# Performance work log

Measured on AMD Instinct MI355X. Metric: run time of the kernel, lower is better.

The kernel has to match this reference:

```python
import jax, jax.numpy as jnp
import numpy as np
import math

D_MODEL = 1024
NUM_HEADS = 16
D_K = D_MODEL // NUM_HEADS  # 64
THETA = 10000.0
B, S = 2, 2048


def setup_inputs() -> dict:
    key = jax.random.key(0)
    kx, kq, kk, kv, ko = jax.random.split(key, 5)
    sigma = (2.0 / (D_MODEL + D_MODEL)) ** 0.5
    return {
        "x": jax.random.normal(kx, (B, S, D_MODEL), dtype=jnp.float32),
        "Wq": jax.random.normal(kq, (D_MODEL, D_MODEL), dtype=jnp.float32) * sigma,
        "Wk": jax.random.normal(kk, (D_MODEL, D_MODEL), dtype=jnp.float32) * sigma,
        "Wv": jax.random.normal(kv, (D_MODEL, D_MODEL), dtype=jnp.float32) * sigma,
        "Wo": jax.random.normal(ko, (D_MODEL, D_MODEL), dtype=jnp.float32) * sigma,
        "token_positions": jnp.arange(S, dtype=jnp.int32),
    }


def _rope(x, token_positions):
    # x: [..., seq, d_k]; rotate interleaved even/odd pairs.
    half = x.shape[-1] // 2
    freq = jnp.power(THETA, -jnp.arange(0, x.shape[-1], 2, dtype=jnp.float32) / x.shape[-1])  # [half]
    angles = token_positions[:, None].astype(jnp.float32) * freq[None, :]  # [seq, half]
    cos, sin = jnp.cos(angles), jnp.sin(angles)
    x1 = x[..., 0::2]
    x2 = x[..., 1::2]
    out = jnp.stack([x1 * cos - x2 * sin, x1 * sin + x2 * cos], axis=-1)  # [..., seq, half, 2]
    return out.reshape(x.shape)


def reference(x, Wq, Wk, Wv, Wo, token_positions):
    Bb, Ss, Dm = x.shape
    H, Dk = NUM_HEADS, D_K
    # Linear: y = x @ W.T ; split as (n head) -> heads first
    def heads(y):
        return y.reshape(Bb, Ss, H, Dk).transpose(0, 2, 1, 3)  # [B,H,S,Dk]
    Q = heads(x @ Wq.T)
    K = heads(x @ Wk.T)
    V = heads(x @ Wv.T)
    Q = _rope(Q, token_positions)
    K = _rope(K, token_positions)
    scores = jnp.einsum("bhqd,bhkd->bhqk", Q, K) / math.sqrt(Dk)  # [B,H,S,S]
    causal = jnp.tril(jnp.ones((Ss, Ss), dtype=bool))
    scores = jnp.where(causal, scores, -jnp.inf)
    # original casts to fp64 for softmax; numerically-stable fp32 softmax here
    probs = jax.nn.softmax(scores, axis=-1)
    attn = jnp.einsum("bhqk,bhkd->bhqd", probs, V)  # [B,H,S,Dk]
    attn = attn.transpose(0, 2, 1, 3).reshape(Bb, Ss, Dm)
    return attn @ Wo.T
```

## Files before the change

kernel.cpp:

```cpp
#include <hip/hip_runtime.h>
#include <hip/hip_bf16.h>
#include <math.h>

typedef __bf16 bf16_t;
typedef __attribute__((ext_vector_type(8))) __bf16 bf16x8;
typedef __attribute__((ext_vector_type(4))) __bf16 bf16x4;
typedef __attribute__((ext_vector_type(4))) float f32x4;

#define B_DIM 2
#define S_DIM 2048
#define H_DIM 16
#define DK 64
#define DM 1024
#define KDIM 1024

#define MFMA(a, b, c) __builtin_amdgcn_mfma_f32_16x16x32_bf16((a), (b), (c), 0, 0, 0)

__device__ __forceinline__ void gload_lds16(const bf16_t* g, bf16_t* l) {
    __builtin_amdgcn_global_load_lds(
        (const __attribute__((address_space(1))) void*)g,
        (__attribute__((address_space(3))) void*)l, 16, 0, 0);
}

__global__ void cvt_all(const float* __restrict__ x,
                        const float* __restrict__ wq, const float* __restrict__ wk,
                        const float* __restrict__ wv, const float* __restrict__ wo,
                        bf16_t* __restrict__ xb,
                        bf16_t* __restrict__ wqb, bf16_t* __restrict__ wkb,
                        bf16_t* __restrict__ wvb, bf16_t* __restrict__ wob) {
    const long NX = (long)B_DIM * S_DIM * DM;
    const long i = ((long)blockIdx.x * 256 + threadIdx.x) * 4;
    const float* s; bf16_t* d; long off;
    if (i < NX) { s = x; d = xb; off = i; }
    else {
        const long j = i - NX;
        const int wsel = (int)(j >> 20);
        off = j & ((1L << 20) - 1);
        switch (wsel) {
            case 0: s = wq; d = wqb; break;
            case 1: s = wk; d = wkb; break;
            case 2: s = wv; d = wvb; break;
            default: s = wo; d = wob; break;
        }
    }
    float4 v = *reinterpret_cast<const float4*>(s + off);
    bf16x4 o;
    o[0] = (__bf16)v.x; o[1] = (__bf16)v.y; o[2] = (__bf16)v.z; o[3] = (__bf16)v.w;
    *reinterpret_cast<bf16x4*>(d + off) = o;
}

template <int MODE>
__global__ __launch_bounds__(256)
void gemm_bt(const bf16_t* __restrict__ A,
             const bf16_t* __restrict__ B0,
             const bf16_t* __restrict__ B1,
             const bf16_t* __restrict__ B2,
             bf16_t* __restrict__ outQ,
             bf16_t* __restrict__ outK,
             bf16_t* __restrict__ outVt,
             float* __restrict__ outF,
             const int* __restrict__ pos) {
    constexpr int CP = 136;
    constexpr int SELEMS = (MODE == 0) ? (128 * CP) : 16384;
    __shared__ bf16_t smem[SELEMS];
    bf16_t* As = smem;
    bf16_t* Bs = smem + 8192;
    bf16_t* Cs = smem;

    const int t = threadIdx.x;
    const int z = blockIdx.z;
    const bf16_t* Bm = (MODE == 0) ? (z == 0 ? B0 : (z == 1 ? B1 : B2)) : B0;

    const int m0 = blockIdx.x * 128;
    const int n0 = blockIdx.y * 128;
    const int lane = t & 63;
    const int w = t >> 6;
    const int wr = w >> 1;
    const int wc = w & 1;

    f32x4 acc[4][4] = {};

    const bf16_t* Ag = A + (size_t)m0 * KDIM;
    const bf16_t* Bg = Bm + (size_t)n0 * KDIM;

    const int rr = lane & 15;
    const int ko = (lane >> 4) * 8;

    int rI[4], cI[4];
#pragma unroll
    for (int c = 0; c < 4; ++c) {
        const int i = t + c * 256;
        rI[c] = i >> 3;
        cI[c] = ((i & 7) ^ (rI[c] & 7)) * 8;
    }

    for (int k0 = 0; k0 < KDIM; k0 += 64) {
#pragma unroll
        for (int c = 0; c < 4; ++c) {
            const int i = t + c * 256;
            gload_lds16(Ag + (size_t)rI[c] * KDIM + k0 + cI[c], &As[i * 8]);
        }
#pragma unroll
        for (int c = 0; c < 4; ++c) {
            const int i = t + c * 256;
            gload_lds16(Bg + (size_t)rI[c] * KDIM + k0 + cI[c], &Bs[i * 8]);
        }
        __syncthreads();

        bf16x8 af[2][4], bfr[2][4];
#pragma unroll
        for (int kk = 0; kk < 2; ++kk) {
#pragma unroll
            for (int m = 0; m < 4; ++m) {
                const int r = wr * 64 + m * 16 + rr;
                af[kk][m] = *reinterpret_cast<const bf16x8*>(
                    &As[r * 64 + ((kk * 32 + ko) ^ ((r & 7) * 8))]);
            }
#pragma unroll
            for (int n = 0; n < 4; ++n) {
                const int r = wc * 64 + n * 16 + rr;
                bfr[kk][n] = *reinterpret_cast<const bf16x8*>(
                    &Bs[r * 64 + ((kk * 32 + ko) ^ ((r & 7) * 8))]);
            }
        }
        __builtin_amdgcn_s_setprio(1);
#pragma unroll
        for (int kk = 0; kk < 2; ++kk)
#pragma unroll
            for (int m = 0; m < 4; ++m)
#pragma unroll
                for (int n = 0; n < 4; ++n)
                    acc[m][n] = MFMA(af[kk][m], bfr[kk][n], acc[m][n]);
        __builtin_amdgcn_s_setprio(0);
        __syncthreads();
    }

    const int rlb = wr * 64 + (lane >> 4) * 4;
    const int clb = wc * 64 + (lane & 15);

    if (MODE == 0) {
        if (z < 2) {
#pragma unroll
            for (int m = 0; m < 4; ++m)
#pragma unroll
                for (int n = 0; n < 4; ++n)
#pragma unroll
                    for (int j = 0; j < 4; ++j)
                        Cs[(rlb + m * 16 + j) * CP + clb + n * 16] = (__bf16)acc[m][n][j];
            __syncthreads();

            bf16_t* dst = (z == 0) ? outQ : outK;
            const int dch = t & 7;
            const int srow = t >> 3;
            float fr[4];
#pragma unroll
            for (int i = 0; i < 4; ++i)
                fr[i] = exp2f((float)(dch * 4 + i) * -0.4152410118609203f);
#pragma unroll
            for (int p = 0; p < 4; ++p) {
                const int s_loc = p * 32 + srow;
                const int gm = m0 + s_loc;
                const int bb = gm >> 11, sg = gm & (S_DIM - 1);
                const float pv = (float)pos[sg];
                float csv[4], snv[4];
#pragma unroll
                for (int i = 0; i < 4; ++i) {
                    const float a = pv * fr[i];
                    csv[i] = cosf(a); snv[i] = sinf(a);
                }
#pragma unroll
                for (int hc = 0; hc < 2; ++hc) {
                    const bf16x8 vv = *reinterpret_cast<const bf16x8*>(
                        &Cs[s_loc * CP + hc * 64 + dch * 8]);
                    bf16x8 ov;
#pragma unroll
                    for (int i = 0; i < 4; ++i) {
                        const float v0 = (float)vv[2 * i], v1 = (float)vv[2 * i + 1];
                        ov[2 * i]     = (__bf16)(v0 * csv[i] - v1 * snv[i]);
                        ov[2 * i + 1] = (__bf16)(v0 * snv[i] + v1 * csv[i]);
                    }
                    const int h = (n0 >> 6) + hc;
                    *reinterpret_cast<bf16x8*>(
                        &dst[((size_t)(bb * H_DIM + h) * S_DIM + sg) * 64 + dch * 8]) = ov;
                }
            }
        } else {
#pragma unroll
            for (int m = 0; m < 4; ++m)
#pragma unroll
                for (int n = 0; n < 4; ++n) {
                    const int cl = clb + n * 16;
                    bf16x4 v4;
#pragma unroll
                    for (int j = 0; j < 4; ++j) v4[j] = (__bf16)acc[m][n][j];
                    *reinterpret_cast<bf16x4*>(&Cs[cl * CP + rlb + m * 16]) = v4;
                }
            __syncthreads();

            const int cl = t >> 1, sh = t & 1;
            const int cg = n0 + cl, h = cg >> 6, d = cg & 63;
            const int bb = m0 >> 11, s0g = m0 & (S_DIM - 1);
            bf16_t* vdst = &outVt[((size_t)(bb * H_DIM + h) * DK + d) * S_DIM + s0g + sh * 64];
#pragma unroll
            for (int i = 0; i < 8; ++i)
                *reinterpret_cast<bf16x8*>(&vdst[i * 8]) =
                    *reinterpret_cast<const bf16x8*>(&Cs[cl * CP + sh * 64 + i * 8]);
        }
    } else {
        const int rbase = m0 + rlb;
        const int cbase = n0 + clb;
#pragma unroll
        for (int m = 0; m < 4; ++m)
#pragma unroll
            for (int n = 0; n < 4; ++n)
#pragma unroll
                for (int j = 0; j < 4; ++j)
                    outF[(size_t)(rbase + m * 16 + j) * DM + cbase + n * 16] = acc[m][n][j];
    }
}

__global__ __launch_bounds__(512, 4)
void attn_kernel(const bf16_t* __restrict__ Q, const bf16_t* __restrict__ Kg,
                 const bf16_t* __restrict__ Vt, bf16_t* __restrict__ O) {
    constexpr int PSTR = 72;
    __shared__ bf16_t Ks[2][64 * 64];
    __shared__ bf16_t Vs[2][64 * 64];
    __shared__ bf16_t P_lds[8][16 * PSTR];

    const int t = threadIdx.x;
    const int lane = t & 63;
    const int w = t >> 6;
    const int bh = blockIdx.x >> 4;
    const int qi = blockIdx.x & 15;
    const int qbH = 31 - qi, qbL = qi;
    const int qbC = (w < 4) ? qbH : qbL;
    const int q0 = qbC * 64 + (w & 3) * 16;
    const int b = bh >> 4, h = bh & 15;
    const int rr = lane & 15;
    const int hi = lane >> 4;

    const bf16_t* Kbh = Kg + (size_t)bh * S_DIM * DK;
    const bf16_t* Vbh = Vt + (size_t)bh * DK * S_DIM;
    bf16_t* Pw = P_lds[w];

    const int r0 = t >> 3, c0 = ((t & 7) ^ (r0 & 7)) * 8;

    const float QSCALE = 0.18033688011112042f;
    const bf16_t* Qp = Q + ((size_t)bh * S_DIM + q0) * DK;
    bf16x8 qf[2];
    qf[0] = *reinterpret_cast<const bf16x8*>(&Qp[rr * DK + hi * 8]);
    qf[1] = *reinterpret_cast<const bf16x8*>(&Qp[rr * DK + 32 + hi * 8]);
#pragma unroll
    for (int i = 0; i < 8; ++i) {
        qf[0][i] = (__bf16)((float)qf[0][i] * QSCALE);
        qf[1][i] = (__bf16)((float)qf[1][i] * QSCALE);
    }

    bf16x8 ones;
#pragma unroll
    for (int i = 0; i < 8; ++i) ones[i] = (__bf16)1.0f;

    f32x4 o[4] = {};
    f32x4 la = {};
    float m = -INFINITY;

    const int ntH = qbH + 1;

    gload_lds16(Kbh + (size_t)r0 * DK + c0, &Ks[0][t * 8]);
    gload_lds16(Vbh + (size_t)r0 * S_DIM + c0, &Vs[0][t * 8]);
    __syncthreads();

    for (int tt = 0; tt < ntH; ++tt) {
        const int cur = tt & 1;
        const int kv0 = tt * 64;

        if (tt + 1 < ntH) {
            const int kv1 = kv0 + 64;
            gload_lds16(Kbh + (size_t)(kv1 + r0) * DK + c0, &Ks[cur ^ 1][t * 8]);
            gload_lds16(Vbh + (size_t)r0 * S_DIM + kv1 + c0, &Vs[cur ^ 1][t * 8]);
        }
        const bf16_t* Kc = Ks[cur];
        const bf16_t* Vc = Vs[cur];

        if (tt <= qbC) {
            f32x4 s[4] = {};
            __builtin_amdgcn_s_setprio(1);
#pragma unroll
            for (int t16 = 0; t16 < 4; ++t16) {
                const int r = t16 * 16 + rr;
                const int sw = (r & 7) * 8;
                bf16x8 kf0 = *reinterpret_cast<const bf16x8*>(&Kc[r * 64 + ((hi * 8) ^ sw)]);
                bf16x8 kf1 = *reinterpret_cast<const bf16x8*>(&Kc[r * 64 + ((32 + hi * 8) ^ sw)]);
                s[t16] = MFMA(kf0, qf[0], s[t16]);
                s[t16] = MFMA(kf1, qf[1], s[t16]);
            }
            __builtin_amdgcn_s_setprio(0);

            if (tt == qbC) {
                const int qg = q0 + rr;
#pragma unroll
                for (int t16 = 0; t16 < 4; ++t16)
#pragma unroll
                    for (int j = 0; j < 4; ++j)
                        if (kv0 + t16 * 16 + hi * 4 + j > qg) s[t16][j] = -INFINITY;
            }

            f32x4 mv = s[0];
#pragma unroll
            for (int t16 = 1; t16 < 4; ++t16) {
                mv[0] = fmaxf(mv[0], s[t16][0]); mv[1] = fmaxf(mv[1], s[t16][1]);
                mv[2] = fmaxf(mv[2], s[t16][2]); mv[3] = fmaxf(mv[3], s[t16][3]);
            }
            const float mloc = fmaxf(fmaxf(mv[0], mv[1]), fmaxf(mv[2], mv[3]));
            if (__any(mloc - m > 8.0f)) {
                float mf = fmaxf(mloc, __shfl_xor(mloc, 16));
                mf = fmaxf(mf, __shfl_xor(mf, 32));
                const float mnew = fmaxf(m, mf);
                const float scale = exp2f(m - mnew);
#pragma unroll
                for (int i = 0; i < 4; ++i) la[i] *= scale;
#pragma unroll
                for (int db = 0; db < 4; ++db)
#pragma unroll
                    for (int j = 0; j < 4; ++j) o[db][j] *= scale;
                m = mnew;
            }
#pragma unroll
            for (int t16 = 0; t16 < 4; ++t16) {
                bf16x4 pb;
#pragma unroll
                for (int j = 0; j < 4; ++j) pb[j] = (__bf16)exp2f(s[t16][j] - m);
                *reinterpret_cast<bf16x4*>(&Pw[rr * PSTR + t16 * 16 + hi * 4]) = pb;
            }

            bf16x8 pf0 = *reinterpret_cast<const bf16x8*>(&Pw[rr * PSTR + hi * 8]);
            bf16x8 pf1 = *reinterpret_cast<const bf16x8*>(&Pw[rr * PSTR + 32 + hi * 8]);
            __builtin_amdgcn_s_setprio(1);
            la = MFMA(ones, pf0, la);
            la = MFMA(ones, pf1, la);
#pragma unroll
            for (int db = 0; db < 4; ++db) {
                const int vr = db * 16 + rr;
                const int sw = (vr & 7) * 8;
                bf16x8 vf0 = *reinterpret_cast<const bf16x8*>(&Vc[vr * 64 + ((hi * 8) ^ sw)]);
                bf16x8 vf1 = *reinterpret_cast<const bf16x8*>(&Vc[vr * 64 + ((32 + hi * 8) ^ sw)]);
                o[db] = MFMA(vf0, pf0, o[db]);
                o[db] = MFMA(vf1, pf1, o[db]);
            }
            __builtin_amdgcn_s_setprio(0);
        }

        __syncthreads();
    }

    const float linv = 1.0f / la[0];
#pragma unroll
    for (int db = 0; db < 4; ++db) {
        bf16x4 ov;
#pragma unroll
        for (int j = 0; j < 4; ++j) ov[j] = (__bf16)(o[db][j] * linv);
        *reinterpret_cast<bf16x4*>(
            &O[((size_t)(b * S_DIM + q0 + rr)) * DM + h * DK + db * 16 + hi * 4]) = ov;
    }
}

extern "C" void kernel_launch(void* const* d_in, const int* in_sizes, int n_in,
                              void* d_out, int out_size, void* d_ws, size_t ws_size,
                              hipStream_t stream) {
    const float* x  = (const float*)d_in[0];
    const float* Wq = (const float*)d_in[1];
    const float* Wk = (const float*)d_in[2];
    const float* Wv = (const float*)d_in[3];
    const float* Wo = (const float*)d_in[4];
    const int* pos  = (const int*)d_in[5];
    float* out = (float*)d_out;

    char* ws = (char*)d_ws;
    bf16_t* xb  = (bf16_t*)(ws);
    bf16_t* Wqb = (bf16_t*)(ws + (8u << 20));
    bf16_t* Wkb = (bf16_t*)(ws + (10u << 20));
    bf16_t* Wvb = (bf16_t*)(ws + (12u << 20));
    bf16_t* Wob = (bf16_t*)(ws + (14u << 20));
    bf16_t* Qb  = (bf16_t*)(ws + (16u << 20));
    bf16_t* Kb  = (bf16_t*)(ws + (24u << 20));
    bf16_t* Vtb = (bf16_t*)(ws + (32u << 20));
    bf16_t* Ab  = (bf16_t*)(ws);

    const int NX = B_DIM * S_DIM * DM;
    const int NW = DM * DM;
    const int NTOT = NX + 4 * NW;

    cvt_all<<<NTOT / 1024, 256, 0, stream>>>(x, Wq, Wk, Wv, Wo,
                                             xb, Wqb, Wkb, Wvb, Wob);

    gemm_bt<0><<<dim3(32, 8, 3), 256, 0, stream>>>(xb, Wqb, Wkb, Wvb,
                                                   Qb, Kb, Vtb, nullptr, pos);

    attn_kernel<<<B_DIM * H_DIM * 16, 512, 0, stream>>>(Qb, Kb, Vtb, Ab);

    gemm_bt<1><<<dim3(32, 8, 1), 256, 0, stream>>>(Ab, Wob, nullptr, nullptr,
                                                   nullptr, nullptr, nullptr, out, pos);
}
```

Baseline: 113.9 us.

## Replace paired causal q-blocks with one q-block per 256-thread workgroup, heavy-first order

```diff
diff --git a/kernel.cpp b/kernel.cpp
--- a/kernel.cpp
+++ b/kernel.cpp
@@ -219,31 +219,32 @@
     }
 }
 
-__global__ __launch_bounds__(512, 4)
+__global__ __launch_bounds__(256, 4)
 void attn_kernel(const bf16_t* __restrict__ Q, const bf16_t* __restrict__ Kg,
                  const bf16_t* __restrict__ Vt, bf16_t* __restrict__ O) {
-    constexpr int PSTR = 72;
     __shared__ bf16_t Ks[2][64 * 64];
     __shared__ bf16_t Vs[2][64 * 64];
-    __shared__ bf16_t P_lds[8][16 * PSTR];
+    __shared__ bf16_t P_lds[4][16 * 64];
 
     const int t = threadIdx.x;
     const int lane = t & 63;
     const int w = t >> 6;
-    const int bh = blockIdx.x >> 4;
-    const int qi = blockIdx.x & 15;
-    const int qbH = 31 - qi, qbL = qi;
-    const int qbC = (w < 4) ? qbH : qbL;
-    const int q0 = qbC * 64 + (w & 3) * 16;
+    const int qbo = blockIdx.x >> 5;
+    const int qb = 31 - qbo;
+    const int bh = blockIdx.x & 31;
+    const int q0 = qb * 64 + w * 16;
     const int b = bh >> 4, h = bh & 15;
     const int rr = lane & 15;
     const int hi = lane >> 4;
+    const int psw = (rr & 7) * 8;
 
     const bf16_t* Kbh = Kg + (size_t)bh * S_DIM * DK;
     const bf16_t* Vbh = Vt + (size_t)bh * DK * S_DIM;
     bf16_t* Pw = P_lds[w];
 
-    const int r0 = t >> 3, c0 = ((t & 7) ^ (r0 & 7)) * 8;
+    const int i0 = t, i1 = t + 256;
+    const int r0 = i0 >> 3, c0 = ((i0 & 7) ^ (r0 & 7)) * 8;
+    const int r1 = i1 >> 3, c1 = ((i1 & 7) ^ (r1 & 7)) * 8;
 
     const float QSCALE = 0.18033688011112042f;
     const bf16_t* Qp = Q + ((size_t)bh * S_DIM + q0) * DK;
@@ -264,91 +265,95 @@
     f32x4 la = {};
     float m = -INFINITY;
 
-    const int ntH = qbH + 1;
-
-    gload_lds16(Kbh + (size_t)r0 * DK + c0, &Ks[0][t * 8]);
-    gload_lds16(Vbh + (size_t)r0 * S_DIM + c0, &Vs[0][t * 8]);
+    const int nt = qb + 1;
+
+    gload_lds16(Kbh + (size_t)r0 * DK + c0, &Ks[0][i0 * 8]);
+    gload_lds16(Kbh + (size_t)r1 * DK + c1, &Ks[0][i1 * 8]);
+    gload_lds16(Vbh + (size_t)r0 * S_DIM + c0, &Vs[0][i0 * 8]);
+    gload_lds16(Vbh + (size_t)r1 * S_DIM + c1, &Vs[0][i1 * 8]);
     __syncthreads();
 
-    for (int tt = 0; tt < ntH; ++tt) {
+    for (int tt = 0; tt < nt; ++tt) {
         const int cur = tt & 1;
         const int kv0 = tt * 64;
 
-        if (tt + 1 < ntH) {
+        if (tt + 1 < nt) {
             const int kv1 = kv0 + 64;
-            gload_lds16(Kbh + (size_t)(kv1 + r0) * DK + c0, &Ks[cur ^ 1][t * 8]);
-            gload_lds16(Vbh + (size_t)r0 * S_DIM + kv1 + c0, &Vs[cur ^ 1][t * 8]);
+            bf16_t* Kn = Ks[cur ^ 1];
+            bf16_t* Vn = Vs[cur ^ 1];
+            gload_lds16(Kbh + (size_t)(kv1 + r0) * DK + c0, &Kn[i0 * 8]);
+            gload_lds16(Kbh + (size_t)(kv1 + r1) * DK + c1, &Kn[i1 * 8]);
+            gload_lds16(Vbh + (size_t)r0 * S_DIM + kv1 + c0, &Vn[i0 * 8]);
+            gload_lds16(Vbh + (size_t)r1 * S_DIM + kv1 + c1, &Vn[i1 * 8]);
         }
         const bf16_t* Kc = Ks[cur];
         const bf16_t* Vc = Vs[cur];
 
-        if (tt <= qbC) {
-            f32x4 s[4] = {};
-            __builtin_amdgcn_s_setprio(1);
-#pragma unroll
-            for (int t16 = 0; t16 < 4; ++t16) {
-                const int r = t16 * 16 + rr;
-                const int sw = (r & 7) * 8;
-                bf16x8 kf0 = *reinterpret_cast<const bf16x8*>(&Kc[r * 64 + ((hi * 8) ^ sw)]);
-                bf16x8 kf1 = *reinterpret_cast<const bf16x8*>(&Kc[r * 64 + ((32 + hi * 8) ^ sw)]);
-                s[t16] = MFMA(kf0, qf[0], s[t16]);
-                s[t16] = MFMA(kf1, qf[1], s[t16]);
-            }
-            __builtin_amdgcn_s_setprio(0);
-
-            if (tt == qbC) {
-                const int qg = q0 + rr;
-#pragma unroll
-                for (int t16 = 0; t16 < 4; ++t16)
-#pragma unroll
-                    for (int j = 0; j < 4; ++j)
-                        if (kv0 + t16 * 16 + hi * 4 + j > qg) s[t16][j] = -INFINITY;
-            }
-
-            f32x4 mv = s[0];
-#pragma unroll
-            for (int t16 = 1; t16 < 4; ++t16) {
-                mv[0] = fmaxf(mv[0], s[t16][0]); mv[1] = fmaxf(mv[1], s[t16][1]);
-                mv[2] = fmaxf(mv[2], s[t16][2]); mv[3] = fmaxf(mv[3], s[t16][3]);
-            }
-            const float mloc = fmaxf(fmaxf(mv[0], mv[1]), fmaxf(mv[2], mv[3]));
-            if (__any(mloc - m > 8.0f)) {
-                float mf = fmaxf(mloc, __shfl_xor(mloc, 16));
-                mf = fmaxf(mf, __shfl_xor(mf, 32));
-                const float mnew = fmaxf(m, mf);
-                const float scale = exp2f(m - mnew);
-#pragma unroll
-                for (int i = 0; i < 4; ++i) la[i] *= scale;
-#pragma unroll
-                for (int db = 0; db < 4; ++db)
-#pragma unroll
-                    for (int j = 0; j < 4; ++j) o[db][j] *= scale;
-                m = mnew;
-            }
-#pragma unroll
-            for (int t16 = 0; t16 < 4; ++t16) {
-                bf16x4 pb;
-#pragma unroll
-                for (int j = 0; j < 4; ++j) pb[j] = (__bf16)exp2f(s[t16][j] - m);
-                *reinterpret_cast<bf16x4*>(&Pw[rr * PSTR + t16 * 16 + hi * 4]) = pb;
-            }
-
-            bf16x8 pf0 = *reinterpret_cast<const bf16x8*>(&Pw[rr * PSTR + hi * 8]);
-            bf16x8 pf1 = *reinterpret_cast<const bf16x8*>(&Pw[rr * PSTR + 32 + hi * 8]);
-            __builtin_amdgcn_s_setprio(1);
-            la = MFMA(ones, pf0, la);
-            la = MFMA(ones, pf1, la);
-#pragma unroll
-            for (int db = 0; db < 4; ++db) {
-                const int vr = db * 16 + rr;
-                const int sw = (vr & 7) * 8;
-                bf16x8 vf0 = *reinterpret_cast<const bf16x8*>(&Vc[vr * 64 + ((hi * 8) ^ sw)]);
-                bf16x8 vf1 = *reinterpret_cast<const bf16x8*>(&Vc[vr * 64 + ((32 + hi * 8) ^ sw)]);
-                o[db] = MFMA(vf0, pf0, o[db]);
-                o[db] = MFMA(vf1, pf1, o[db]);
-            }
-            __builtin_amdgcn_s_setprio(0);
-        }
+        f32x4 s[4] = {};
+        __builtin_amdgcn_s_setprio(1);
+#pragma unroll
+        for (int t16 = 0; t16 < 4; ++t16) {
+            const int r = t16 * 16 + rr;
+            const int sw = (r & 7) * 8;
+            bf16x8 kf0 = *reinterpret_cast<const bf16x8*>(&Kc[r * 64 + ((hi * 8) ^ sw)]);
+            bf16x8 kf1 = *reinterpret_cast<const bf16x8*>(&Kc[r * 64 + ((32 + hi * 8) ^ sw)]);
+            s[t16] = MFMA(kf0, qf[0], s[t16]);
+            s[t16] = MFMA(kf1, qf[1], s[t16]);
+        }
+        __builtin_amdgcn_s_setprio(0);
+
+        if (tt == qb) {
+            const int qg = q0 + rr;
+#pragma unroll
+            for (int t16 = 0; t16 < 4; ++t16)
+#pragma unroll
+                for (int j = 0; j < 4; ++j)
+                    if (kv0 + t16 * 16 + hi * 4 + j > qg) s[t16][j] = -INFINITY;
+        }
+
+        f32x4 mv = s[0];
+#pragma unroll
+        for (int t16 = 1; t16 < 4; ++t16) {
+            mv[0] = fmaxf(mv[0], s[t16][0]); mv[1] = fmaxf(mv[1], s[t16][1]);
+            mv[2] = fmaxf(mv[2], s[t16][2]); mv[3] = fmaxf(mv[3], s[t16][3]);
+        }
+        const float mloc = fmaxf(fmaxf(mv[0], mv[1]), fmaxf(mv[2], mv[3]));
+        if (__any(mloc - m > 8.0f)) {
+            float mf = fmaxf(mloc, __shfl_xor(mloc, 16));
+            mf = fmaxf(mf, __shfl_xor(mf, 32));
+            const float mnew = fmaxf(m, mf);
+            const float scale = exp2f(m - mnew);
+#pragma unroll
+            for (int i = 0; i < 4; ++i) la[i] *= scale;
+#pragma unroll
+            for (int db = 0; db < 4; ++db)
+#pragma unroll
+                for (int j = 0; j < 4; ++j) o[db][j] *= scale;
+            m = mnew;
+        }
+#pragma unroll
+        for (int t16 = 0; t16 < 4; ++t16) {
+            bf16x4 pb;
+#pragma unroll
+            for (int j = 0; j < 4; ++j) pb[j] = (__bf16)exp2f(s[t16][j] - m);
+            *reinterpret_cast<bf16x4*>(&Pw[rr * 64 + ((t16 * 16 + hi * 4) ^ psw)]) = pb;
+        }
+
+        bf16x8 pf0 = *reinterpret_cast<const bf16x8*>(&Pw[rr * 64 + ((hi * 8) ^ psw)]);
+        bf16x8 pf1 = *reinterpret_cast<const bf16x8*>(&Pw[rr * 64 + ((32 + hi * 8) ^ psw)]);
+        __builtin_amdgcn_s_setprio(1);
+        la = MFMA(ones, pf0, la);
+        la = MFMA(ones, pf1, la);
+#pragma unroll
+        for (int db = 0; db < 4; ++db) {
+            const int vr = db * 16 + rr;
+            const int sw = (vr & 7) * 8;
+            bf16x8 vf0 = *reinterpret_cast<const bf16x8*>(&Vc[vr * 64 + ((hi * 8) ^ sw)]);
+            bf16x8 vf1 = *reinterpret_cast<const bf16x8*>(&Vc[vr * 64 + ((32 + hi * 8) ^ sw)]);
+            o[db] = MFMA(vf0, pf0, o[db]);
+            o[db] = MFMA(vf1, pf1, o[db]);
+        }
+        __builtin_amdgcn_s_setprio(0);
 
         __syncthreads();
     }
@@ -396,7 +401,7 @@
     gemm_bt<0><<<dim3(32, 8, 3), 256, 0, stream>>>(xb, Wqb, Wkb, Wvb,
                                                    Qb, Kb, Vtb, nullptr, pos);
 
-    attn_kernel<<<B_DIM * H_DIM * 16, 512, 0, stream>>>(Qb, Kb, Vtb, Ab);
+    attn_kernel<<<B_DIM * H_DIM * 32, 256, 0, stream>>>(Qb, Kb, Vtb, Ab);
 
     gemm_bt<1><<<dim3(32, 8, 1), 256, 0, stream>>>(Ab, Wob, nullptr, nullptr,
                                                    nullptr, nullptr, nullptr, out, pos);
```

Measured after the change: 110.0 us, median of 2. -3.4%, faster.

## Switch attention blocks to contiguous 128-row query tiles with XOR-swizzled P buffer

Applied to the files above, without the earlier changes.

```diff
diff --git a/kernel.cpp b/kernel.cpp
--- a/kernel.cpp
+++ b/kernel.cpp
@@ -219,25 +219,25 @@
     }
 }
 
-__global__ __launch_bounds__(512, 4)
+__global__ __launch_bounds__(512, 3)
 void attn_kernel(const bf16_t* __restrict__ Q, const bf16_t* __restrict__ Kg,
                  const bf16_t* __restrict__ Vt, bf16_t* __restrict__ O) {
-    constexpr int PSTR = 72;
     __shared__ bf16_t Ks[2][64 * 64];
     __shared__ bf16_t Vs[2][64 * 64];
-    __shared__ bf16_t P_lds[8][16 * PSTR];
+    __shared__ bf16_t P_lds[8][16 * 64];
 
     const int t = threadIdx.x;
     const int lane = t & 63;
     const int w = t >> 6;
-    const int bh = blockIdx.x >> 4;
-    const int qi = blockIdx.x & 15;
-    const int qbH = 31 - qi, qbL = qi;
-    const int qbC = (w < 4) ? qbH : qbL;
-    const int q0 = qbC * 64 + (w & 3) * 16;
+    const int qBo = blockIdx.x >> 5;
+    const int qB = 15 - qBo;
+    const int bh = blockIdx.x & 31;
+    const int q0 = qB * 128 + w * 16;
+    const int qbw = q0 >> 6;
     const int b = bh >> 4, h = bh & 15;
     const int rr = lane & 15;
     const int hi = lane >> 4;
+    const int psw = (rr & 7) * 8;
 
     const bf16_t* Kbh = Kg + (size_t)bh * S_DIM * DK;
     const bf16_t* Vbh = Vt + (size_t)bh * DK * S_DIM;
@@ -264,17 +264,17 @@
     f32x4 la = {};
     float m = -INFINITY;
 
-    const int ntH = qbH + 1;
+    const int nt = 2 * qB + 2;
 
     gload_lds16(Kbh + (size_t)r0 * DK + c0, &Ks[0][t * 8]);
     gload_lds16(Vbh + (size_t)r0 * S_DIM + c0, &Vs[0][t * 8]);
     __syncthreads();
 
-    for (int tt = 0; tt < ntH; ++tt) {
+    for (int tt = 0; tt < nt; ++tt) {
         const int cur = tt & 1;
         const int kv0 = tt * 64;
 
-        if (tt + 1 < ntH) {
+        if (tt + 1 < nt) {
             const int kv1 = kv0 + 64;
             gload_lds16(Kbh + (size_t)(kv1 + r0) * DK + c0, &Ks[cur ^ 1][t * 8]);
             gload_lds16(Vbh + (size_t)r0 * S_DIM + kv1 + c0, &Vs[cur ^ 1][t * 8]);
@@ -282,7 +282,7 @@
         const bf16_t* Kc = Ks[cur];
         const bf16_t* Vc = Vs[cur];
 
-        if (tt <= qbC) {
+        if (tt <= qbw) {
             f32x4 s[4] = {};
             __builtin_amdgcn_s_setprio(1);
 #pragma unroll
@@ -296,7 +296,7 @@
             }
             __builtin_amdgcn_s_setprio(0);
 
-            if (tt == qbC) {
+            if (tt == qbw) {
                 const int qg = q0 + rr;
 #pragma unroll
                 for (int t16 = 0; t16 < 4; ++t16)
@@ -330,11 +330,11 @@
                 bf16x4 pb;
 #pragma unroll
                 for (int j = 0; j < 4; ++j) pb[j] = (__bf16)exp2f(s[t16][j] - m);
-                *reinterpret_cast<bf16x4*>(&Pw[rr * PSTR + t16 * 16 + hi * 4]) = pb;
-            }
-
-            bf16x8 pf0 = *reinterpret_cast<const bf16x8*>(&Pw[rr * PSTR + hi * 8]);
-            bf16x8 pf1 = *reinterpret_cast<const bf16x8*>(&Pw[rr * PSTR + 32 + hi * 8]);
+                *reinterpret_cast<bf16x4*>(&Pw[rr * 64 + ((t16 * 16 + hi * 4) ^ psw)]) = pb;
+            }
+
+            bf16x8 pf0 = *reinterpret_cast<const bf16x8*>(&Pw[rr * 64 + ((hi * 8) ^ psw)]);
+            bf16x8 pf1 = *reinterpret_cast<const bf16x8*>(&Pw[rr * 64 + ((32 + hi * 8) ^ psw)]);
             __builtin_amdgcn_s_setprio(1);
             la = MFMA(ones, pf0, la);
             la = MFMA(ones, pf1, la);
```

Measured after the change: 117.3 us. 1.03x slower.
